# Optimization experiments

Hardware: AMD Instinct MI355X
Metric: run time of the kernel (lower is better)

## Reference

```python
import jax, jax.numpy as jnp
import numpy as np

LN_EPS = 1e-5

def _layernorm_2d(x):
    # nn.LayerNorm([64, 16]) with default (identity) affine: normalize jointly
    # over the last two axes (biased variance, eps=1e-5).
    m = jnp.mean(x, axis=(-2, -1), keepdims=True)
    v = jnp.mean(jnp.square(x - m), axis=(-2, -1), keepdims=True)
    return (x - m) * jax.lax.rsqrt(v + LN_EPS)

def setup_inputs() -> dict:
    key = jax.random.key(0)
    ks = jax.random.split(key, 8)
    B, P, D = 32768, 64, 16
    x = jax.random.normal(ks[0], (B, P, D), dtype=jnp.float32)
    # attention params: torch.randn init in the source
    Wq = jax.random.normal(ks[1], (D, D), dtype=jnp.float32)
    Wk = jax.random.normal(ks[2], (D, D), dtype=jnp.float32)
    Wv = jax.random.normal(ks[3], (D, D), dtype=jnp.float32)
    # 64 independent 2-layer MLPs (Linear(16,16) each), batched as grouped weights.
    # torch Linear default init: U(-1/sqrt(fan_in), 1/sqrt(fan_in))
    bound = 1.0 / np.sqrt(D)
    W1 = jax.random.uniform(ks[4], (P, D, D), jnp.float32, -bound, bound)
    b1 = jax.random.uniform(ks[5], (P, D), jnp.float32, -bound, bound)
    W2 = jax.random.uniform(ks[6], (P, D, D), jnp.float32, -bound, bound)
    b2 = jax.random.uniform(ks[7], (P, D), jnp.float32, -bound, bound)
    return {"x": x, "Wq": Wq, "Wk": Wk, "Wv": Wv,
            "W1": W1, "b1": b1, "W2": W2, "b2": b2}

def reference(x, Wq, Wk, Wv, W1, b1, W2, b2):
    # --- tiny self-attention, temperature 3 ---
    Q = x @ Wq          # [B, 64, 16]
    K = x @ Wk
    V = x @ Wv
    scores = jnp.einsum('bqd,bkd->bqk', Q, K) / 3.0   # [B, 64, 64]
    # NOTE: the source calls F.softmax with no dim on a 3-D tensor; PyTorch's
    # deprecated implicit-dim rule picks dim=0 (the batch axis). Faithful here.
    attn = jax.nn.softmax(scores, axis=0)
    z = jnp.einsum('bqk,bkd->bqd', attn, V)
    x = _layernorm_2d(x + z)
    y = x
    # --- 64 independent per-patch MLPs, collapsed into grouped matmuls ---
    h = jax.nn.relu(jnp.einsum('bpi,pio->bpo', x, W1) + b1)
    h = jax.nn.relu(jnp.einsum('bpi,pio->bpo', h, W2) + b2)
    return _layernorm_2d(h + y)
```

## Files before the change

kernel.cpp:

```cpp
#include <hip/hip_runtime.h>
#include <stdint.h>
#include <math.h>


__device__ __forceinline__ float rdlane_f(float v, int srclane) {
    return __uint_as_float((unsigned)__builtin_amdgcn_readlane((int)__float_as_uint(v), srclane));
}
__device__ __forceinline__ float bf16_lo(unsigned u) { return __uint_as_float(u << 16); }
__device__ __forceinline__ float bf16_hi(unsigned u) { return __uint_as_float(u & 0xffff0000u); }

__global__ void k0_prep(const float* __restrict__ Wq, const float* __restrict__ Wk,
                        const float* __restrict__ W1, const float* __restrict__ W2,
                        float* __restrict__ G, unsigned short* __restrict__ W1h,
                        unsigned short* __restrict__ W2h)
{
    const int t = threadIdx.x;
    {
        const int i = t >> 4, j = t & 15;
        float acc = 0.f;
        #pragma unroll
        for (int d = 0; d < 16; ++d) acc = fmaf(Wq[i*16 + d], Wk[j*16 + d], acc);
        G[i*16 + j] = acc * (1.0f / 3.0f);
    }
    for (int idx = t; idx < 16384; idx += 256) {
        const unsigned u1 = __float_as_uint(W1[idx]);
        W1h[idx] = (unsigned short)((u1 + 0x7fffu + ((u1 >> 16) & 1u)) >> 16);
        const unsigned u2 = __float_as_uint(W2[idx]);
        W2h[idx] = (unsigned short)((u2 + 0x7fffu + ((u2 >> 16) & 1u)) >> 16);
    }
}

__global__ __launch_bounds__(256, 2) void k1_stats(
    const float* __restrict__ x, const float* __restrict__ G,
    float* __restrict__ pm, float* __restrict__ ps, int batches_per_block)
{
    const int lane = threadIdx.x & 63;
    const int w    = threadIdx.x >> 6;

    float m_r[16], s_r[16];
    #pragma unroll
    for (int kk = 0; kk < 16; ++kk) { m_r[kk] = -INFINITY; s_r[kk] = 0.f; }

    const size_t b0 = (size_t)blockIdx.x * batches_per_block;
    for (int bi = 0; bi < batches_per_block; ++bi) {
        const float* xb = x + (b0 + bi) * 1024 + lane * 16;
        float xr[16];
        #pragma unroll
        for (int c = 0; c < 4; ++c) {
            const float4 v = *(const float4*)(xb + 4*c);
            xr[4*c+0] = v.x; xr[4*c+1] = v.y; xr[4*c+2] = v.z; xr[4*c+3] = v.w;
        }
        float U[16];
        #pragma unroll
        for (int j = 0; j < 16; ++j) U[j] = 0.f;
        #pragma unroll
        for (int i = 0; i < 16; ++i) {
            const float xi = xr[i];
            #pragma unroll
            for (int j = 0; j < 16; ++j) U[j] = fmaf(xi, G[i*16 + j], U[j]);
        }
        #pragma unroll
        for (int kk = 0; kk < 16; ++kk) {
            const int k = (w << 4) + kk;
            float s = 0.f;
            #pragma unroll
            for (int i = 0; i < 16; ++i) s = fmaf(rdlane_f(xr[i], k), U[i], s);
            if (s <= m_r[kk]) {
                s_r[kk] += __expf(s - m_r[kk]);
            } else {
                s_r[kk] = fmaf(s_r[kk], __expf(m_r[kk] - s), 1.0f);
                m_r[kk] = s;
            }
        }
    }
    float* pmb = pm + (size_t)blockIdx.x * 4096;
    float* psb = ps + (size_t)blockIdx.x * 4096;
    #pragma unroll
    for (int kk = 0; kk < 16; ++kk) {
        const int k = (w << 4) + kk;
        pmb[k*64 + lane] = m_r[kk];
        psb[k*64 + lane] = s_r[kk];
    }
}

__global__ void k2_reduce(const float* __restrict__ pm, const float* __restrict__ ps,
                          float* __restrict__ LT, int nblocks)
{
    const int tid = blockIdx.x * 256 + threadIdx.x;
    float m = -INFINITY, s = 0.f;
    for (int blk = 0; blk < nblocks; ++blk) {
        const float mb = pm[(size_t)blk * 4096 + tid];
        const float sb = ps[(size_t)blk * 4096 + tid];
        if (mb <= m) {
            s += sb * __expf(mb - m);
        } else {
            s = fmaf(s, __expf(m - mb), sb);
            m = mb;
        }
    }
    LT[tid] = m + __logf(s);
}

__global__ __launch_bounds__(256, 2) void k3_main(
    const float* __restrict__ x, const float* __restrict__ G,
    const float* __restrict__ Wv, const float* __restrict__ LT,
    const unsigned short* __restrict__ W1h, const float* __restrict__ b1,
    const unsigned short* __restrict__ W2h, const float* __restrict__ b2,
    float* __restrict__ out, int batches_per_block)
{
    __shared__ float zp[4][64][17];
    __shared__ float y_lds[64][17];
    __shared__ float h_lds[64][17];
    __shared__ float red1[4][2];
    __shared__ float red2[4][2];

    const int lane = threadIdx.x & 63;
    const int w    = threadIdx.x >> 6;
    const int o0   = w << 2;

    uint2 w1r[16], w2r[16];
    const uint2* W1v = (const uint2*)W1h;
    const uint2* W2v = (const uint2*)W2h;
    #pragma unroll
    for (int i = 0; i < 16; ++i) {
        const int eo = (lane*256 + i*16 + o0) >> 2;
        w1r[i] = W1v[eo];
        w2r[i] = W2v[eo];
    }
    const float4 b1r = *(const float4*)(b1 + lane*16 + o0);
    const float4 b2r = *(const float4*)(b2 + lane*16 + o0);

    for (int bi = 0; bi < batches_per_block; ++bi) {
        const size_t b = (size_t)blockIdx.x * batches_per_block + bi;
        const float* xb = x + b * 1024;

        float xr[16];
        #pragma unroll
        for (int c = 0; c < 4; ++c) {
            const float4 v = *(const float4*)(xb + lane*16 + 4*c);
            xr[4*c+0] = v.x; xr[4*c+1] = v.y; xr[4*c+2] = v.z; xr[4*c+3] = v.w;
        }
        float U[16], V[16];
        #pragma unroll
        for (int j = 0; j < 16; ++j) { U[j] = 0.f; V[j] = 0.f; }
        #pragma unroll
        for (int i = 0; i < 16; ++i) {
            const float xi = xr[i];
            #pragma unroll
            for (int j = 0; j < 16; ++j) {
                U[j] = fmaf(xi, G[i*16 + j],  U[j]);
                V[j] = fmaf(xi, Wv[i*16 + j], V[j]);
            }
        }
        float z[16];
        #pragma unroll
        for (int d = 0; d < 16; ++d) z[d] = 0.f;
        #pragma unroll
        for (int kk = 0; kk < 16; ++kk) {
            const int k = (w << 4) + kk;
            float s = 0.f;
            #pragma unroll
            for (int i = 0; i < 16; ++i) s = fmaf(rdlane_f(xr[i], k), U[i], s);
            const float p = __expf(s - LT[k*64 + lane]);
            #pragma unroll
            for (int d = 0; d < 16; ++d) z[d] = fmaf(p, rdlane_f(V[d], k), z[d]);
        }
        #pragma unroll
        for (int d = 0; d < 16; ++d) zp[w][lane][d] = z[d];
        __syncthreads();

        float tv[4];
        {
            const float4 xre = *(const float4*)(xb + lane*16 + o0);
            const float xs[4] = {xre.x, xre.y, xre.z, xre.w};
            #pragma unroll
            for (int j = 0; j < 4; ++j)
                tv[j] = zp[0][lane][o0+j] + zp[1][lane][o0+j]
                      + zp[2][lane][o0+j] + zp[3][lane][o0+j] + xs[j];
        }
        float sm = tv[0] + tv[1] + tv[2] + tv[3];
        float sq = fmaf(tv[0], tv[0], fmaf(tv[1], tv[1], fmaf(tv[2], tv[2], tv[3]*tv[3])));
        #pragma unroll
        for (int off = 1; off < 64; off <<= 1) {
            sm += __shfl_xor(sm, off);
            sq += __shfl_xor(sq, off);
        }
        if (lane == 0) { red1[w][0] = sm; red1[w][1] = sq; }
        __syncthreads();
        {
            const float S  = red1[0][0] + red1[1][0] + red1[2][0] + red1[3][0];
            const float SS = red1[0][1] + red1[1][1] + red1[2][1] + red1[3][1];
            const float mean = S * (1.f/1024.f);
            const float var  = SS * (1.f/1024.f) - mean*mean;
            const float rinv = rsqrtf(var + 1e-5f);
            #pragma unroll
            for (int j = 0; j < 4; ++j) y_lds[lane][o0+j] = (tv[j] - mean) * rinv;
        }
        __syncthreads();

        float yrow[16];
        #pragma unroll
        for (int i = 0; i < 16; ++i) yrow[i] = y_lds[lane][i];
        float h0 = b1r.x, h1 = b1r.y, h2 = b1r.z, h3 = b1r.w;
        #pragma unroll
        for (int i = 0; i < 16; ++i) {
            const float yi = yrow[i];
            const uint2 ww = w1r[i];
            h0 = fmaf(yi, bf16_lo(ww.x), h0);
            h1 = fmaf(yi, bf16_hi(ww.x), h1);
            h2 = fmaf(yi, bf16_lo(ww.y), h2);
            h3 = fmaf(yi, bf16_hi(ww.y), h3);
        }
        h0 = fmaxf(h0, 0.f); h1 = fmaxf(h1, 0.f); h2 = fmaxf(h2, 0.f); h3 = fmaxf(h3, 0.f);
        h_lds[lane][o0+0] = h0; h_lds[lane][o0+1] = h1;
        h_lds[lane][o0+2] = h2; h_lds[lane][o0+3] = h3;
        __syncthreads();

        float hrow[16];
        #pragma unroll
        for (int i = 0; i < 16; ++i) hrow[i] = h_lds[lane][i];
        float g0 = b2r.x, g1 = b2r.y, g2 = b2r.z, g3 = b2r.w;
        #pragma unroll
        for (int i = 0; i < 16; ++i) {
            const float hi = hrow[i];
            const uint2 ww = w2r[i];
            g0 = fmaf(hi, bf16_lo(ww.x), g0);
            g1 = fmaf(hi, bf16_hi(ww.x), g1);
            g2 = fmaf(hi, bf16_lo(ww.y), g2);
            g3 = fmaf(hi, bf16_hi(ww.y), g3);
        }
        g0 = fmaxf(g0, 0.f); g1 = fmaxf(g1, 0.f); g2 = fmaxf(g2, 0.f); g3 = fmaxf(g3, 0.f);

        float sv[4];
        sv[0] = g0 + y_lds[lane][o0+0];
        sv[1] = g1 + y_lds[lane][o0+1];
        sv[2] = g2 + y_lds[lane][o0+2];
        sv[3] = g3 + y_lds[lane][o0+3];
        float sm2 = sv[0] + sv[1] + sv[2] + sv[3];
        float sq2 = fmaf(sv[0], sv[0], fmaf(sv[1], sv[1], fmaf(sv[2], sv[2], sv[3]*sv[3])));
        #pragma unroll
        for (int off = 1; off < 64; off <<= 1) {
            sm2 += __shfl_xor(sm2, off);
            sq2 += __shfl_xor(sq2, off);
        }
        if (lane == 0) { red2[w][0] = sm2; red2[w][1] = sq2; }
        __syncthreads();
        {
            const float S  = red2[0][0] + red2[1][0] + red2[2][0] + red2[3][0];
            const float SS = red2[0][1] + red2[1][1] + red2[2][1] + red2[3][1];
            const float mean = S * (1.f/1024.f);
            const float var  = SS * (1.f/1024.f) - mean*mean;
            const float rinv = rsqrtf(var + 1e-5f);
            float4 ov;
            ov.x = (sv[0] - mean) * rinv;
            ov.y = (sv[1] - mean) * rinv;
            ov.z = (sv[2] - mean) * rinv;
            ov.w = (sv[3] - mean) * rinv;
            *(float4*)(out + b*1024 + lane*16 + o0) = ov;
        }
        __syncthreads();
    }
}

extern "C" void kernel_launch(void* const* d_in, const int* in_sizes, int n_in,
                              void* d_out, int out_size, void* d_ws, size_t ws_size,
                              hipStream_t stream)
{
    const float* x  = (const float*)d_in[0];
    const float* Wq = (const float*)d_in[1];
    const float* Wk = (const float*)d_in[2];
    const float* Wv = (const float*)d_in[3];
    const float* W1 = (const float*)d_in[4];
    const float* b1 = (const float*)d_in[5];
    const float* W2 = (const float*)d_in[6];
    const float* b2 = (const float*)d_in[7];
    float* out = (float*)d_out;

    char* ws = (char*)d_ws;
    float*          G   = (float*)(ws);
    unsigned short* W1h = (unsigned short*)(ws + 1024);
    unsigned short* W2h = (unsigned short*)(ws + 1024 + 32768);
    float*          LT  = (float*)(ws + 1024 + 65536);
    const size_t    off_pm = 131072;

    int k1_blocks = 512;
    const size_t per_block_bytes = 4096 * 2 * sizeof(float);
    while (k1_blocks > 1 && off_pm + (size_t)k1_blocks * per_block_bytes > ws_size)
        k1_blocks >>= 1;
    const int k1_bpb = 32768 / k1_blocks;
    float* pm = (float*)(ws + off_pm);
    float* ps = pm + (size_t)k1_blocks * 4096;

    k0_prep <<<1,    256, 0, stream>>>(Wq, Wk, W1, W2, G, W1h, W2h);
    k1_stats<<<k1_blocks, 256, 0, stream>>>(x, G, pm, ps, k1_bpb);
    k2_reduce<<<16,  256, 0, stream>>>(pm, ps, LT, k1_blocks);
    k3_main <<<1024, 256, 0, stream>>>(x, G, Wv, LT, W1h, b1, W2h, b2, out, 32);
}
```

Before: 3.095 ms.

## Replace readlane score loops with LDS-staged x/U/V and split U/V across waves

Each wave now computes only its 4-column slice of U=xG and V=xWv using weights staged in LDS. The slices are shared through LDS, and the score and z loops read neighbour rows as float4 from LDS instead of issuing 32 scalar readlanes per key. LT values are preloaded into registers and the trailing barrier in k3 is dropped. k2 gets 4-way independent accumulators, k1 uses more blocks, and launch bounds are raised. This trades readlane serialization and redundant full-width U/V compute for extra LDS traffic and barriers. Dropping the barrier relies on the double-buffered or aliased LDS regions staying correct.

```diff
diff --git a/kernel.cpp b/kernel.cpp
--- a/kernel.cpp
+++ b/kernel.cpp
@@ -3,9 +3,6 @@
 #include <math.h>
 
 
-__device__ __forceinline__ float rdlane_f(float v, int srclane) {
-    return __uint_as_float((unsigned)__builtin_amdgcn_readlane((int)__float_as_uint(v), srclane));
-}
 __device__ __forceinline__ float bf16_lo(unsigned u) { return __uint_as_float(u << 16); }
 __device__ __forceinline__ float bf16_hi(unsigned u) { return __uint_as_float(u & 0xffff0000u); }
 
@@ -30,41 +27,60 @@
     }
 }
 
-__global__ __launch_bounds__(256, 2) void k1_stats(
+__global__ __launch_bounds__(256, 4) void k1_stats(
     const float* __restrict__ x, const float* __restrict__ G,
     float* __restrict__ pm, float* __restrict__ ps, int batches_per_block)
 {
-    const int lane = threadIdx.x & 63;
-    const int w    = threadIdx.x >> 6;
+    __shared__ float G_lds[256];
+    __shared__ float xb_lds[2][1024];
+    __shared__ float U_lds[2][1280];
+
+    const int t = threadIdx.x, lane = t & 63, w = t >> 6, o0 = w << 2;
+    if (t < 64) ((float4*)G_lds)[t] = ((const float4*)G)[t];
 
     float m_r[16], s_r[16];
     #pragma unroll
     for (int kk = 0; kk < 16; ++kk) { m_r[kk] = -INFINITY; s_r[kk] = 0.f; }
+    __syncthreads();
 
     const size_t b0 = (size_t)blockIdx.x * batches_per_block;
     for (int bi = 0; bi < batches_per_block; ++bi) {
-        const float* xb = x + (b0 + bi) * 1024 + lane * 16;
+        const float* xb = x + (b0 + bi) * 1024;
+        float* xl = xb_lds[bi & 1];
+        float* Ul = U_lds[bi & 1];
+        ((float4*)xl)[t] = ((const float4*)xb)[t];
         float xr[16];
         #pragma unroll
         for (int c = 0; c < 4; ++c) {
-            const float4 v = *(const float4*)(xb + 4*c);
+            const float4 v = ((const float4*)(xb + lane*16))[c];
             xr[4*c+0] = v.x; xr[4*c+1] = v.y; xr[4*c+2] = v.z; xr[4*c+3] = v.w;
         }
-        float U[16];
-        #pragma unroll
-        for (int j = 0; j < 16; ++j) U[j] = 0.f;
+        float u0 = 0.f, u1 = 0.f, u2 = 0.f, u3 = 0.f;
         #pragma unroll
         for (int i = 0; i < 16; ++i) {
-            const float xi = xr[i];
-            #pragma unroll
-            for (int j = 0; j < 16; ++j) U[j] = fmaf(xi, G[i*16 + j], U[j]);
+            const float4 g = *(const float4*)&G_lds[i*16 + o0];
+            u0 = fmaf(xr[i], g.x, u0); u1 = fmaf(xr[i], g.y, u1);
+            u2 = fmaf(xr[i], g.z, u2); u3 = fmaf(xr[i], g.w, u3);
+        }
+        *(float4*)&Ul[lane*20 + o0] = make_float4(u0, u1, u2, u3);
+        __syncthreads();
+        float Ur[16];
+        #pragma unroll
+        for (int c = 0; c < 4; ++c) {
+            const float4 uu = *(const float4*)&Ul[lane*20 + 4*c];
+            Ur[4*c+0] = uu.x; Ur[4*c+1] = uu.y; Ur[4*c+2] = uu.z; Ur[4*c+3] = uu.w;
         }
         #pragma unroll
         for (int kk = 0; kk < 16; ++kk) {
             const int k = (w << 4) + kk;
-            float s = 0.f;
+            float s0 = 0.f, s1 = 0.f, s2 = 0.f, s3 = 0.f;
             #pragma unroll
-            for (int i = 0; i < 16; ++i) s = fmaf(rdlane_f(xr[i], k), U[i], s);
+            for (int c = 0; c < 4; ++c) {
+                const float4 xv = *(const float4*)&xl[k*16 + 4*c];
+                s0 = fmaf(xv.x, Ur[4*c+0], s0); s1 = fmaf(xv.y, Ur[4*c+1], s1);
+                s2 = fmaf(xv.z, Ur[4*c+2], s2); s3 = fmaf(xv.w, Ur[4*c+3], s3);
+            }
+            const float s = (s0 + s1) + (s2 + s3);
             if (s <= m_r[kk]) {
                 s_r[kk] += __expf(s - m_r[kk]);
             } else {
@@ -87,36 +103,56 @@
                           float* __restrict__ LT, int nblocks)
 {
     const int tid = blockIdx.x * 256 + threadIdx.x;
-    float m = -INFINITY, s = 0.f;
-    for (int blk = 0; blk < nblocks; ++blk) {
+    float m[4], s[4];
+    #pragma unroll
+    for (int u = 0; u < 4; ++u) { m[u] = -INFINITY; s[u] = 0.f; }
+    int blk = 0;
+    for (; blk + 4 <= nblocks; blk += 4) {
+        #pragma unroll
+        for (int u = 0; u < 4; ++u) {
+            const float mb = pm[(size_t)(blk + u) * 4096 + tid];
+            const float sb = ps[(size_t)(blk + u) * 4096 + tid];
+            if (mb <= m[u]) {
+                s[u] += sb * __expf(mb - m[u]);
+            } else {
+                s[u] = fmaf(s[u], __expf(m[u] - mb), sb);
+                m[u] = mb;
+            }
+        }
+    }
+    for (; blk < nblocks; ++blk) {
         const float mb = pm[(size_t)blk * 4096 + tid];
         const float sb = ps[(size_t)blk * 4096 + tid];
-        if (mb <= m) {
-            s += sb * __expf(mb - m);
-        } else {
-            s = fmaf(s, __expf(m - mb), sb);
-            m = mb;
-        }
-    }
-    LT[tid] = m + __logf(s);
-}
-
-__global__ __launch_bounds__(256, 2) void k3_main(
+        if (mb <= m[0]) { s[0] += sb * __expf(mb - m[0]); }
+        else { s[0] = fmaf(s[0], __expf(m[0] - mb), sb); m[0] = mb; }
+    }
+    #pragma unroll
+    for (int u = 1; u < 4; ++u) {
+        if (m[u] <= m[0]) { s[0] += s[u] * __expf(m[u] - m[0]); }
+        else { s[0] = fmaf(s[0], __expf(m[0] - m[u]), s[u]); m[0] = m[u]; }
+    }
+    LT[tid] = m[0] + __logf(s[0]);
+}
+
+__global__ __launch_bounds__(256, 3) void k3_main(
     const float* __restrict__ x, const float* __restrict__ G,
     const float* __restrict__ Wv, const float* __restrict__ LT,
     const unsigned short* __restrict__ W1h, const float* __restrict__ b1,
     const unsigned short* __restrict__ W2h, const float* __restrict__ b2,
     float* __restrict__ out, int batches_per_block)
 {
-    __shared__ float zp[4][64][17];
-    __shared__ float y_lds[64][17];
-    __shared__ float h_lds[64][17];
+    __shared__ float G_lds[256];
+    __shared__ float Wv_lds[256];
+    __shared__ float x_lds[1024];
+    __shared__ float U_lds[1280];
+    __shared__ float V_lds[1280];
+    __shared__ float zp_lds[5120];
     __shared__ float red1[4][2];
     __shared__ float red2[4][2];
 
-    const int lane = threadIdx.x & 63;
-    const int w    = threadIdx.x >> 6;
-    const int o0   = w << 2;
+    const int t = threadIdx.x, lane = t & 63, w = t >> 6, o0 = w << 2;
+    if (t < 64)       ((float4*)G_lds)[t]        = ((const float4*)G)[t];
+    else if (t < 128) ((float4*)Wv_lds)[t - 64]  = ((const float4*)Wv)[t - 64];
 
     uint2 w1r[16], w2r[16];
     const uint2* W1v = (const uint2*)W1h;
@@ -129,28 +165,41 @@
     }
     const float4 b1r = *(const float4*)(b1 + lane*16 + o0);
     const float4 b2r = *(const float4*)(b2 + lane*16 + o0);
+    float LTr[16];
+    #pragma unroll
+    for (int kk = 0; kk < 16; ++kk) LTr[kk] = LT[((w << 4) + kk)*64 + lane];
+    __syncthreads();
 
     for (int bi = 0; bi < batches_per_block; ++bi) {
         const size_t b = (size_t)blockIdx.x * batches_per_block + bi;
         const float* xb = x + b * 1024;
-
+        ((float4*)x_lds)[t] = ((const float4*)xb)[t];
         float xr[16];
         #pragma unroll
         for (int c = 0; c < 4; ++c) {
-            const float4 v = *(const float4*)(xb + lane*16 + 4*c);
+            const float4 v = ((const float4*)(xb + lane*16))[c];
             xr[4*c+0] = v.x; xr[4*c+1] = v.y; xr[4*c+2] = v.z; xr[4*c+3] = v.w;
         }
-        float U[16], V[16];
-        #pragma unroll
-        for (int j = 0; j < 16; ++j) { U[j] = 0.f; V[j] = 0.f; }
+        float u0=0.f,u1=0.f,u2=0.f,u3=0.f, v0=0.f,v1=0.f,v2=0.f,v3=0.f;
         #pragma unroll
         for (int i = 0; i < 16; ++i) {
+            const float4 g  = *(const float4*)&G_lds[i*16 + o0];
+            const float4 wv = *(const float4*)&Wv_lds[i*16 + o0];
             const float xi = xr[i];
-            #pragma unroll
-            for (int j = 0; j < 16; ++j) {
-                U[j] = fmaf(xi, G[i*16 + j],  U[j]);
-                V[j] = fmaf(xi, Wv[i*16 + j], V[j]);
-            }
+            u0 = fmaf(xi, g.x,  u0); u1 = fmaf(xi, g.y,  u1);
+            u2 = fmaf(xi, g.z,  u2); u3 = fmaf(xi, g.w,  u3);
+            v0 = fmaf(xi, wv.x, v0); v1 = fmaf(xi, wv.y, v1);
+            v2 = fmaf(xi, wv.z, v2); v3 = fmaf(xi, wv.w, v3);
+        }
+        *(float4*)&U_lds[lane*20 + o0] = make_float4(u0,u1,u2,u3);
+        *(float4*)&V_lds[lane*20 + o0] = make_float4(v0,v1,v2,v3);
+        __syncthreads();
+
+        float Ur[16];
+        #pragma unroll
+        for (int c = 0; c < 4; ++c) {
+            const float4 uu = *(const float4*)&U_lds[lane*20 + 4*c];
+            Ur[4*c+0] = uu.x; Ur[4*c+1] = uu.y; Ur[4*c+2] = uu.z; Ur[4*c+3] = uu.w;
         }
         float z[16];
         #pragma unroll
@@ -158,25 +207,39 @@
         #pragma unroll
         for (int kk = 0; kk < 16; ++kk) {
             const int k = (w << 4) + kk;
-            float s = 0.f;
+            float s0=0.f,s1=0.f,s2=0.f,s3=0.f;
             #pragma unroll
-            for (int i = 0; i < 16; ++i) s = fmaf(rdlane_f(xr[i], k), U[i], s);
-            const float p = __expf(s - LT[k*64 + lane]);
+            for (int c = 0; c < 4; ++c) {
+                const float4 xv = *(const float4*)&x_lds[k*16 + 4*c];
+                s0 = fmaf(xv.x, Ur[4*c+0], s0); s1 = fmaf(xv.y, Ur[4*c+1], s1);
+                s2 = fmaf(xv.z, Ur[4*c+2], s2); s3 = fmaf(xv.w, Ur[4*c+3], s3);
+            }
+            const float s = (s0 + s1) + (s2 + s3);
+            const float p = __expf(s - LTr[kk]);
             #pragma unroll
-            for (int d = 0; d < 16; ++d) z[d] = fmaf(p, rdlane_f(V[d], k), z[d]);
-        }
-        #pragma unroll
-        for (int d = 0; d < 16; ++d) zp[w][lane][d] = z[d];
+            for (int c = 0; c < 4; ++c) {
+                const float4 vv = *(const float4*)&V_lds[k*20 + 4*c];
+                z[4*c+0] = fmaf(p, vv.x, z[4*c+0]); z[4*c+1] = fmaf(p, vv.y, z[4*c+1]);
+                z[4*c+2] = fmaf(p, vv.z, z[4*c+2]); z[4*c+3] = fmaf(p, vv.w, z[4*c+3]);
+            }
+        }
+        #pragma unroll
+        for (int c = 0; c < 4; ++c)
+            *(float4*)&zp_lds[w*1280 + lane*20 + 4*c] =
+                make_float4(z[4*c+0], z[4*c+1], z[4*c+2], z[4*c+3]);
         __syncthreads();
 
         float tv[4];
         {
-            const float4 xre = *(const float4*)(xb + lane*16 + o0);
-            const float xs[4] = {xre.x, xre.y, xre.z, xre.w};
-            #pragma unroll
-            for (int j = 0; j < 4; ++j)
-                tv[j] = zp[0][lane][o0+j] + zp[1][lane][o0+j]
-                      + zp[2][lane][o0+j] + zp[3][lane][o0+j] + xs[j];
+            const float4 xre = ((const float4*)(xb + lane*16))[w];
+            const float4 a = *(const float4*)&zp_lds[0*1280 + lane*20 + o0];
+            const float4 bq= *(const float4*)&zp_lds[1*1280 + lane*20 + o0];
+            const float4 cq= *(const float4*)&zp_lds[2*1280 + lane*20 + o0];
+            const float4 dq= *(const float4*)&zp_lds[3*1280 + lane*20 + o0];
+            tv[0] = a.x + bq.x + cq.x + dq.x + xre.x;
+            tv[1] = a.y + bq.y + cq.y + dq.y + xre.y;
+            tv[2] = a.z + bq.z + cq.z + dq.z + xre.z;
+            tv[3] = a.w + bq.w + cq.w + dq.w + xre.w;
         }
         float sm = tv[0] + tv[1] + tv[2] + tv[3];
         float sq = fmaf(tv[0], tv[0], fmaf(tv[1], tv[1], fmaf(tv[2], tv[2], tv[3]*tv[3])));
@@ -193,18 +256,21 @@
             const float mean = S * (1.f/1024.f);
             const float var  = SS * (1.f/1024.f) - mean*mean;
             const float rinv = rsqrtf(var + 1e-5f);
-            #pragma unroll
-            for (int j = 0; j < 4; ++j) y_lds[lane][o0+j] = (tv[j] - mean) * rinv;
-        }
-        __syncthreads();
-
-        float yrow[16];
-        #pragma unroll
-        for (int i = 0; i < 16; ++i) yrow[i] = y_lds[lane][i];
+            *(float4*)&zp_lds[lane*20 + o0] = make_float4(
+                (tv[0]-mean)*rinv, (tv[1]-mean)*rinv, (tv[2]-mean)*rinv, (tv[3]-mean)*rinv);
+        }
+        __syncthreads();
+
+        float yr[16];
+        #pragma unroll
+        for (int c = 0; c < 4; ++c) {
+            const float4 yv = *(const float4*)&zp_lds[lane*20 + 4*c];
+            yr[4*c+0] = yv.x; yr[4*c+1] = yv.y; yr[4*c+2] = yv.z; yr[4*c+3] = yv.w;
+        }
         float h0 = b1r.x, h1 = b1r.y, h2 = b1r.z, h3 = b1r.w;
         #pragma unroll
         for (int i = 0; i < 16; ++i) {
-            const float yi = yrow[i];
+            const float yi = yr[i];
             const uint2 ww = w1r[i];
             h0 = fmaf(yi, bf16_lo(ww.x), h0);
             h1 = fmaf(yi, bf16_hi(ww.x), h1);
@@ -212,17 +278,19 @@
             h3 = fmaf(yi, bf16_hi(ww.y), h3);
         }
         h0 = fmaxf(h0, 0.f); h1 = fmaxf(h1, 0.f); h2 = fmaxf(h2, 0.f); h3 = fmaxf(h3, 0.f);
-        h_lds[lane][o0+0] = h0; h_lds[lane][o0+1] = h1;
-        h_lds[lane][o0+2] = h2; h_lds[lane][o0+3] = h3;
-        __syncthreads();
-
-        float hrow[16];
-        #pragma unroll
-        for (int i = 0; i < 16; ++i) hrow[i] = h_lds[lane][i];
+        *(float4*)&zp_lds[1280 + lane*20 + o0] = make_float4(h0,h1,h2,h3);
+        __syncthreads();
+
+        float hr[16];
+        #pragma unroll
+        for (int c = 0; c < 4; ++c) {
+            const float4 hv = *(const float4*)&zp_lds[1280 + lane*20 + 4*c];
+            hr[4*c+0] = hv.x; hr[4*c+1] = hv.y; hr[4*c+2] = hv.z; hr[4*c+3] = hv.w;
+        }
         float g0 = b2r.x, g1 = b2r.y, g2 = b2r.z, g3 = b2r.w;
         #pragma unroll
         for (int i = 0; i < 16; ++i) {
-            const float hi = hrow[i];
+            const float hi = hr[i];
             const uint2 ww = w2r[i];
             g0 = fmaf(hi, bf16_lo(ww.x), g0);
             g1 = fmaf(hi, bf16_hi(ww.x), g1);
@@ -231,11 +299,9 @@
         }
         g0 = fmaxf(g0, 0.f); g1 = fmaxf(g1, 0.f); g2 = fmaxf(g2, 0.f); g3 = fmaxf(g3, 0.f);
 
+        const float4 yre = *(const float4*)&zp_lds[lane*20 + o0];
         float sv[4];
-        sv[0] = g0 + y_lds[lane][o0+0];
-        sv[1] = g1 + y_lds[lane][o0+1];
-        sv[2] = g2 + y_lds[lane][o0+2];
-        sv[3] = g3 + y_lds[lane][o0+3];
+        sv[0] = g0 + yre.x; sv[1] = g1 + yre.y; sv[2] = g2 + yre.z; sv[3] = g3 + yre.w;
         float sm2 = sv[0] + sv[1] + sv[2] + sv[3];
         float sq2 = fmaf(sv[0], sv[0], fmaf(sv[1], sv[1], fmaf(sv[2], sv[2], sv[3]*sv[3])));
         #pragma unroll
@@ -258,7 +324,6 @@
             ov.w = (sv[3] - mean) * rinv;
             *(float4*)(out + b*1024 + lane*16 + o0) = ov;
         }
-        __syncthreads();
     }
 }
 
@@ -283,9 +348,9 @@
     float*          LT  = (float*)(ws + 1024 + 65536);
     const size_t    off_pm = 131072;
 
-    int k1_blocks = 512;
+    int k1_blocks = 1024;
     const size_t per_block_bytes = 4096 * 2 * sizeof(float);
-    while (k1_blocks > 1 && off_pm + (size_t)k1_blocks * per_block_bytes > ws_size)
+    while (k1_blocks > 4 && off_pm + (size_t)k1_blocks * per_block_bytes > ws_size)
         k1_blocks >>= 1;
     const int k1_bpb = 32768 / k1_blocks;
     float* pm = (float*)(ws + off_pm);
```

Result: faster. 3.012 ms (-2.7%).
